# Kernel tuning notes

Hardware: AMD Instinct MI355X
Metric: run time of the kernel (lower is better)

Reference implementation:

```python
import jax, jax.numpy as jnp
import numpy as np

B, N, PD = 4, 4096, 1024
D, S = 16, 64              # max_span, span_dim
ALL = D * S                # 1024

# fwd[t, tau] = tau - t if 0 <= tau - t < D else D (points at padding slot)
FWD = np.array([[tau - t if 0 <= tau - t < D else D for tau in range(2 * D)]
                for t in range(D)], dtype=np.int32)           # [D, 2D]
BWD = np.array([[t + d for d in range(D)] for t in range(D)], dtype=np.int32)  # [D, D]
T_IDX = np.arange(D, dtype=np.int32)


def _gather(x, idx, padding):
    # x: [B, N, D, S]; pad span dim, reshape seq into blocks of D, gather spans.
    # out[b, n, t, j, s] = x_padded[b, n, t, idx[t, j], s]  -> [B, N//D, D, idx.shape[1], S]
    b, n, d, s = x.shape
    pad = jnp.full((b, n, 1, s), padding, dtype=x.dtype)
    x = jnp.concatenate([x, pad], axis=2).reshape(b, n // d, d, d + 1, s)
    return x[:, :, T_IDX[:, None], idx, :]


def setup_inputs() -> dict:
    key = jax.random.key(0)
    k1, k2, k3, k4, k5 = jax.random.split(key, 5)
    return {
        "x":   jax.random.normal(k1, (B, N, PD), jnp.float32),
        "W_r": jax.random.normal(k2, (PD, 2 * ALL), jnp.float32) * 0.02,
        "b_r": jax.random.normal(k3, (2 * ALL,), jnp.float32) * 0.02,
        "W_w": jax.random.normal(k4, (ALL, PD), jnp.float32) * 0.02,
        "b_w": jax.random.normal(k5, (PD,), jnp.float32) * 0.02,
    }


def reference(x, W_r, b_r, W_w, b_w):
    # reader: Linear(PD -> 2*ALL), split into left/right span logits
    P = (x @ W_r + b_r).reshape(B, N, 2, D, S)
    L = P[:, :, 0]                                  # [B, N, D, S]
    R = jnp.roll(P[:, :, 1], -1, axis=1)            # roll(-1) along seq
    Lg = _gather(L, FWD, -10000.0)                  # [B, T, D, 2D, S]
    Rg = _gather(R, np.roll(FWD, 1, axis=1), 0.0)   # [B, T, D, 2D, S]
    Lg = jnp.transpose(Lg, (0, 1, 4, 2, 3))         # [B, T, S, D, 2D]
    Rg = jnp.transpose(Rg, (0, 1, 4, 2, 3))
    Lg = jax.nn.softmax(Lg, axis=-1)
    L0, L1 = Lg[..., :D], Lg[..., D:]
    R0, R1 = Rg[..., :D], Rg[..., D:]
    Q0 = L0 @ R0                                    # [B, T, S, D, D]
    Q1 = L0 @ R1 + L1 @ jnp.roll(R0, -1, axis=1)
    mask = jnp.ones((Q1.shape[1],), Q1.dtype).at[-1].set(0.0)  # zero last block
    Q1 = Q1 * mask[None, :, None, None, None]
    Q = jnp.concatenate([Q0, Q1], axis=-1)          # [B, T, S, D, 2D]
    Q = jnp.transpose(Q, (0, 1, 3, 4, 2))           # [B, T, D, 2D, S]
    Q = Q[:, :, T_IDX[:, None], BWD, :]             # [B, T, D, D, S]
    out = Q.reshape(B, N, ALL)
    return out @ W_w + b_w                          # writer: Linear(ALL -> PD)
```

## Files before the change

kernel.cpp:

```cpp
#include <hip/hip_runtime.h>
#include <hip/hip_bf16.h>

#define B_ 4
#define N_ 4096
#define PD_ 1024
#define D_ 16
#define S_ 64
#define ALL_ 1024
#define TWOALL_ 2048
#define M_ 16384

typedef __bf16 bf16x8 __attribute__((ext_vector_type(8)));
typedef float floatx4 __attribute__((ext_vector_type(4)));

__device__ __forceinline__ float bf2f(unsigned short u) {
    union { unsigned int i; float f; } v;
    v.i = ((unsigned int)u) << 16;
    return v.f;
}

__device__ __forceinline__ unsigned short f2bf(float f) {
    unsigned int x = __float_as_uint(f);
    unsigned int r = (x + 0x7fffu + ((x >> 16) & 1u)) >> 16;
    return (unsigned short)r;
}

__device__ __forceinline__ void load_lds_16(const void* g, void* l) {
    __builtin_amdgcn_global_load_lds(
        (const __attribute__((address_space(1))) void*)g,
        (__attribute__((address_space(3))) void*)l, 16, 0, 0);
}

__global__ __launch_bounds__(256) void convert_f32_bf16(
    const float* __restrict__ in, unsigned short* __restrict__ out, int n4) {
    int i = blockIdx.x * 256 + threadIdx.x;
    if (i >= n4) return;
    float4 v = *(const float4*)(in + (size_t)i * 4);
    ushort4 o;
    o.x = f2bf(v.x); o.y = f2bf(v.y); o.z = f2bf(v.z); o.w = f2bf(v.w);
    *(ushort4*)(out + (size_t)i * 4) = o;
}

__global__ void transpose_f32_bf16(const float* __restrict__ in,
                                   unsigned short* __restrict__ out,
                                   int rows, int cols) {
    __shared__ float tile[32][33];
    int bx = blockIdx.x * 32;
    int by = blockIdx.y * 32;
    int tx = threadIdx.x;
    int ty = threadIdx.y;
    #pragma unroll
    for (int i = 0; i < 32; i += 8)
        tile[ty + i][tx] = in[(size_t)(by + ty + i) * cols + bx + tx];
    __syncthreads();
    #pragma unroll
    for (int i = 0; i < 32; i += 8)
        out[(size_t)(bx + ty + i) * rows + by + tx] = f2bf(tile[tx][ty + i]);
}

#define BM 256
#define BN 256
#define BK 64

#define STAGE_A(buf_, h_, kt_) do { \
    load_lds_16(a_base + (size_t)((h_) * 128) * K + (kt_) * 64, \
                &As[buf_][((h_) * 128 + wave * 16) * 64]); \
    load_lds_16(a_base + (size_t)((h_) * 128 + 8) * K + (kt_) * 64, \
                &As[buf_][((h_) * 128 + wave * 16 + 8) * 64]); \
  } while (0)

#define STAGE_B(buf_, h_, kt_) do { \
    load_lds_16(b_base + (size_t)((h_) * 128) * K + (kt_) * 64, \
                &Bs[buf_][((h_) * 128 + wave * 16) * 64]); \
    load_lds_16(b_base + (size_t)((h_) * 128 + 8) * K + (kt_) * 64, \
                &Bs[buf_][((h_) * 128 + wave * 16 + 8) * 64]); \
  } while (0)

#define LOAD_AF(mh_) do { \
    _Pragma("unroll") \
    for (int i = 0; i < 4; ++i) { \
        const unsigned short* p_ = Ab + (wm * 128 + (mh_) * 64 + i * 16 + lrow) * 64; \
        af[i][0] = *(const bf16x8*)(p_ + ((g0 ^ (lrow & 7)) * 8)); \
        af[i][1] = *(const bf16x8*)(p_ + (((g0 + 4) ^ (lrow & 7)) * 8)); \
    } } while (0)

#define LOAD_BH(dst_, nh_) do { \
    _Pragma("unroll") \
    for (int j = 0; j < 2; ++j) { \
        const unsigned short* p_ = Bb + (wn * 64 + (nh_) * 32 + j * 16 + lrow) * 64; \
        dst_[j][0] = *(const bf16x8*)(p_ + ((g0 ^ (lrow & 7)) * 8)); \
        dst_[j][1] = *(const bf16x8*)(p_ + (((g0 + 4) ^ (lrow & 7)) * 8)); \
    } } while (0)

#define MMA_Q(mh_, nh_, bq_) do { \
    __builtin_amdgcn_s_setprio(1); \
    _Pragma("unroll") \
    for (int kk = 0; kk < 2; ++kk) \
      _Pragma("unroll") \
      for (int i = 0; i < 4; ++i) \
        _Pragma("unroll") \
        for (int j = 0; j < 2; ++j) \
          acc[(mh_) * 4 + i][(nh_) * 2 + j] = \
              __builtin_amdgcn_mfma_f32_16x16x32_bf16( \
                  af[i][kk], bq_[j][kk], acc[(mh_) * 4 + i][(nh_) * 2 + j], 0, 0, 0); \
    __builtin_amdgcn_s_setprio(0); \
  } while (0)

#define MID_BAR() do { \
    __builtin_amdgcn_sched_barrier(0); \
    __builtin_amdgcn_s_barrier(); \
    asm volatile("s_waitcnt lgkmcnt(0)" ::: "memory"); \
  } while (0)

#define POST_BAR() do { \
    __builtin_amdgcn_s_barrier(); \
    __builtin_amdgcn_sched_barrier(0); \
  } while (0)

template <int OUT_BF>
__global__ __launch_bounds__(512, 2) void gemm_bf16(
    const unsigned short* __restrict__ A,
    const unsigned short* __restrict__ Bt,
    const float* __restrict__ bias,
    void* __restrict__ Cv,
    int M, int N, int K, int gxl, int gypx) {

    __shared__ __align__(16) unsigned short As[2][BM * BK];
    __shared__ __align__(16) unsigned short Bs[2][BN * BK];

    const int tid  = threadIdx.x;
    const int lane = tid & 63;
    const int wave = tid >> 6;
    const int wm   = wave & 1;
    const int wn   = wave >> 1;

    const int flat = blockIdx.x;
    const int xcd  = flat & 7;
    const int slot = flat >> 3;
    const int bx   = slot & ((1 << gxl) - 1);
    const int by   = xcd * gypx + (slot >> gxl);
    const int bm0  = by * BM;
    const int bn0  = bx * BN;

    const int lrow = lane & 15;
    const int g0   = lane >> 4;

    const int srow = lane >> 3;
    const int sg   = (lane & 7) ^ srow;

    const unsigned short* a_base =
        A + (size_t)(bm0 + wave * 16 + srow) * K + sg * 8;
    const unsigned short* b_base =
        Bt + (size_t)(bn0 + wave * 16 + srow) * K + sg * 8;

    floatx4 acc[8][4] = {};
    bf16x8 af[4][2];
    bf16x8 bf0[2][2];
    bf16x8 bf1[2][2];

    const int NTk = K >> 6;

    STAGE_A(0, 0, 0); STAGE_A(0, 1, 0); STAGE_B(0, 0, 0); STAGE_B(0, 1, 0);
    if (NTk > 1) {
        STAGE_A(1, 0, 1); STAGE_A(1, 1, 1); STAGE_B(1, 0, 1);
        asm volatile("s_waitcnt vmcnt(6)" ::: "memory");
    } else {
        asm volatile("s_waitcnt vmcnt(0)" ::: "memory");
    }
    POST_BAR();

    for (int t = 0; t < NTk; ++t) {
        const int buf = t & 1;
        const unsigned short* Ab = As[buf];
        const unsigned short* Bb = Bs[buf];

        LOAD_AF(0);
        LOAD_BH(bf0, 0);
        if (t + 1 < NTk) STAGE_B((t + 1) & 1, 1, t + 1);
        asm volatile("s_waitcnt lgkmcnt(8)" ::: "memory");
        MID_BAR();
        MMA_Q(0, 0, bf0);
        POST_BAR();

        LOAD_BH(bf1, 1);
        MID_BAR();
        MMA_Q(0, 1, bf1);
        POST_BAR();

        LOAD_AF(1);
        if (t + 2 < NTk) STAGE_B(buf, 0, t + 2);
        MID_BAR();
        MMA_Q(1, 1, bf1);
        POST_BAR();

        if (t + 2 < NTk) { STAGE_A(buf, 0, t + 2); STAGE_A(buf, 1, t + 2); }
        __builtin_amdgcn_sched_barrier(0);
        __builtin_amdgcn_s_barrier();
        MMA_Q(1, 0, bf0);
        if (t + 2 < NTk) {
            asm volatile("s_waitcnt vmcnt(6)" ::: "memory");
        } else if (t + 1 < NTk) {
            asm volatile("s_waitcnt vmcnt(0)" ::: "memory");
        }
        POST_BAR();
    }

    #pragma unroll
    for (int n = 0; n < 4; ++n) {
        int col = bn0 + wn * 64 + n * 16 + (lane & 15);
        float bv = bias[col];
        #pragma unroll
        for (int m = 0; m < 8; ++m) {
            #pragma unroll
            for (int r = 0; r < 4; ++r) {
                int row = bm0 + wm * 128 + m * 16 + (lane >> 4) * 4 + r;
                float v = acc[m][n][r] + bv;
                if (OUT_BF)
                    ((unsigned short*)Cv)[(size_t)row * N + col] = f2bf(v);
                else
                    ((float*)Cv)[(size_t)row * N + col] = v;
            }
        }
    }
}

__global__ __launch_bounds__(256) void middle_kernel(
    const unsigned short* __restrict__ P,
    unsigned short* __restrict__ A2) {

    int idx = blockIdx.x * 256 + threadIdx.x;
    int s   = idx & 63;
    int r   = idx >> 6;
    int n   = r & (N_ - 1);
    const int t = n & (D_ - 1);
    const int c = n >> 4;

    const unsigned short* Lp = P + (size_t)r * TWOALL_ + s;
    float w[16];
    float mx = -1e30f;
    #pragma unroll
    for (int j = 0; j < 16; ++j) {
        w[j] = bf2f(Lp[j * S_]);
        mx = fmaxf(mx, w[j]);
    }
    float sum = 0.f;
    #pragma unroll
    for (int j = 0; j < 16; ++j) {
        w[j] = __expf(w[j] - mx);
        sum += w[j];
    }
    float inv = 1.0f / sum;

    float q[16];
    #pragma unroll
    for (int d = 0; d < 16; ++d) q[d] = 0.f;

    #pragma unroll
    for (int i = 0; i < 15; ++i) {
        int np = n + i + 1;
        if (np >= N_) np -= N_;
        int b = r >> 12;
        const unsigned short* Rp = P + (((size_t)(b * N_ + np)) * 2 + 1) * ALL_ + s;
        #pragma unroll
        for (int k = 0; k < 15 - i; ++k) {
            q[i + k + 1] += w[i] * bf2f(Rp[k * S_]);
        }
    }

    unsigned short* out = A2 + (size_t)r * ALL_ + s;
    bool last = (c == (N_ / D_) - 1);
    #pragma unroll
    for (int d = 0; d < 16; ++d) {
        float v = (d == 0) ? 0.f : q[d] * inv;
        if (last && (t + d >= D_)) v = 0.f;
        out[d * S_] = f2bf(v);
    }
}

extern "C" void kernel_launch(void* const* d_in, const int* in_sizes, int n_in,
                              void* d_out, int out_size, void* d_ws, size_t ws_size,
                              hipStream_t stream) {
    const float* x   = (const float*)d_in[0];
    const float* W_r = (const float*)d_in[1];
    const float* b_r = (const float*)d_in[2];
    const float* W_w = (const float*)d_in[3];
    const float* b_w = (const float*)d_in[4];
    float* out = (float*)d_out;

    unsigned short* ws  = (unsigned short*)d_ws;
    unsigned short* P   = ws;
    unsigned short* xbf = P   + (size_t)M_ * TWOALL_;
    unsigned short* A2  = xbf + (size_t)M_ * ALL_;
    unsigned short* WrT = A2  + (size_t)M_ * ALL_;
    unsigned short* WwT = WrT + (size_t)TWOALL_ * PD_;

    convert_f32_bf16<<<dim3((M_ * PD_ / 4 + 255) / 256), 256, 0, stream>>>(
        x, xbf, M_ * PD_ / 4);

    dim3 tb(32, 8);
    transpose_f32_bf16<<<dim3(TWOALL_ / 32, PD_ / 32), tb, 0, stream>>>(W_r, WrT, PD_, TWOALL_);
    transpose_f32_bf16<<<dim3(ALL_ / 32, PD_ / 32), tb, 0, stream>>>(W_w, WwT, PD_, ALL_);

    gemm_bf16<1><<<dim3((TWOALL_ / BN) * (M_ / BM)), 512, 0, stream>>>(
        xbf, WrT, b_r, P, M_, TWOALL_, PD_, 3, (M_ / BM) / 8);

    middle_kernel<<<dim3((B_ * N_ * S_) / 256), 256, 0, stream>>>(P, A2);

    gemm_bf16<0><<<dim3((ALL_ / BN) * (M_ / BM)), 512, 0, stream>>>(
        A2, WwT, b_w, out, M_, ALL_, PD_, 2, (M_ / BM) / 8);
}
```

Baseline: 293.1 us.

## Restructure GEMM main loop prefetch schedule with one-ahead A and two-ahead B staging

Reorders the four MFMA quadrants so the A fragments are reloaded instead of holding two B fragment sets, which cuts register use. A tiles are now prefetched one K-step ahead into the opposite buffer and B tiles two steps ahead. Global and LDS addresses are precomputed as incrementing pointers and fixed offsets, and an extra scheduling barrier is added after the LDS wait. The cost is one additional LDS read of the A fragments per iteration, and the more intricate buffer hazard timing could stall or race.

```diff
diff --git a/kernel.cpp b/kernel.cpp
--- a/kernel.cpp
+++ b/kernel.cpp
@@ -62,47 +62,31 @@
 #define BN 256
 #define BK 64
 
-#define STAGE_A(buf_, h_, kt_) do { \
-    load_lds_16(a_base + (size_t)((h_) * 128) * K + (kt_) * 64, \
-                &As[buf_][((h_) * 128 + wave * 16) * 64]); \
-    load_lds_16(a_base + (size_t)((h_) * 128 + 8) * K + (kt_) * 64, \
-                &As[buf_][((h_) * 128 + wave * 16 + 8) * 64]); \
-  } while (0)
-
-#define STAGE_B(buf_, h_, kt_) do { \
-    load_lds_16(b_base + (size_t)((h_) * 128) * K + (kt_) * 64, \
-                &Bs[buf_][((h_) * 128 + wave * 16) * 64]); \
-    load_lds_16(b_base + (size_t)((h_) * 128 + 8) * K + (kt_) * 64, \
-                &Bs[buf_][((h_) * 128 + wave * 16 + 8) * 64]); \
-  } while (0)
-
 #define LOAD_AF(mh_) do { \
     _Pragma("unroll") \
-    for (int i = 0; i < 4; ++i) { \
-        const unsigned short* p_ = Ab + (wm * 128 + (mh_) * 64 + i * 16 + lrow) * 64; \
-        af[i][0] = *(const bf16x8*)(p_ + ((g0 ^ (lrow & 7)) * 8)); \
-        af[i][1] = *(const bf16x8*)(p_ + (((g0 + 4) ^ (lrow & 7)) * 8)); \
+    for (int i_ = 0; i_ < 4; ++i_) { \
+        af[i_][0] = *(const bf16x8*)(rdA + bufoff + (mh_) * 4096 + i_ * 1024 + cg0); \
+        af[i_][1] = *(const bf16x8*)(rdA + bufoff + (mh_) * 4096 + i_ * 1024 + cg1); \
     } } while (0)
 
-#define LOAD_BH(dst_, nh_) do { \
+#define LOAD_B(nh_) do { \
     _Pragma("unroll") \
-    for (int j = 0; j < 2; ++j) { \
-        const unsigned short* p_ = Bb + (wn * 64 + (nh_) * 32 + j * 16 + lrow) * 64; \
-        dst_[j][0] = *(const bf16x8*)(p_ + ((g0 ^ (lrow & 7)) * 8)); \
-        dst_[j][1] = *(const bf16x8*)(p_ + (((g0 + 4) ^ (lrow & 7)) * 8)); \
+    for (int j_ = 0; j_ < 2; ++j_) { \
+        bq[j_][0] = *(const bf16x8*)(rdB + bufoff + (nh_) * 2048 + j_ * 1024 + cg0); \
+        bq[j_][1] = *(const bf16x8*)(rdB + bufoff + (nh_) * 2048 + j_ * 1024 + cg1); \
     } } while (0)
 
-#define MMA_Q(mh_, nh_, bq_) do { \
+#define MMA_Q(mh_, nh_) do { \
     __builtin_amdgcn_s_setprio(1); \
     _Pragma("unroll") \
     for (int kk = 0; kk < 2; ++kk) \
       _Pragma("unroll") \
-      for (int i = 0; i < 4; ++i) \
+      for (int i_ = 0; i_ < 4; ++i_) \
         _Pragma("unroll") \
-        for (int j = 0; j < 2; ++j) \
-          acc[(mh_) * 4 + i][(nh_) * 2 + j] = \
+        for (int j_ = 0; j_ < 2; ++j_) \
+          acc[(mh_) * 4 + i_][(nh_) * 2 + j_] = \
               __builtin_amdgcn_mfma_f32_16x16x32_bf16( \
-                  af[i][kk], bq_[j][kk], acc[(mh_) * 4 + i][(nh_) * 2 + j], 0, 0, 0); \
+                  af[i_][kk], bq[j_][kk], acc[(mh_) * 4 + i_][(nh_) * 2 + j_], 0, 0, 0); \
     __builtin_amdgcn_s_setprio(0); \
   } while (0)
 
@@ -110,6 +94,7 @@
     __builtin_amdgcn_sched_barrier(0); \
     __builtin_amdgcn_s_barrier(); \
     asm volatile("s_waitcnt lgkmcnt(0)" ::: "memory"); \
+    __builtin_amdgcn_sched_barrier(0); \
   } while (0)
 
 #define POST_BAR() do { \
@@ -153,56 +138,97 @@
     const unsigned short* b_base =
         Bt + (size_t)(bn0 + wave * 16 + srow) * K + sg * 8;
 
+    const int cg0 = (g0 ^ (lrow & 7)) * 8;
+    const int cg1 = cg0 ^ 32;
+    const unsigned short* rdA = &As[0][(wm * 128 + lrow) * 64];
+    const unsigned short* rdB = &Bs[0][(wn * 64  + lrow) * 64];
+
+    const unsigned short* pA0  = a_base + 64;
+    const unsigned short* pA0b = a_base + 64 + (size_t)8   * K;
+    const unsigned short* pA1  = a_base + 64 + (size_t)128 * K;
+    const unsigned short* pA1b = a_base + 64 + (size_t)136 * K;
+    const unsigned short* pB0  = b_base + 128;
+    const unsigned short* pB0b = b_base + 128 + (size_t)8   * K;
+    const unsigned short* pB1  = b_base + 128 + (size_t)128 * K;
+    const unsigned short* pB1b = b_base + 128 + (size_t)136 * K;
+
     floatx4 acc[8][4] = {};
     bf16x8 af[4][2];
-    bf16x8 bf0[2][2];
-    bf16x8 bf1[2][2];
+    bf16x8 bq[2][2];
 
     const int NTk = K >> 6;
 
-    STAGE_A(0, 0, 0); STAGE_A(0, 1, 0); STAGE_B(0, 0, 0); STAGE_B(0, 1, 0);
-    if (NTk > 1) {
-        STAGE_A(1, 0, 1); STAGE_A(1, 1, 1); STAGE_B(1, 0, 1);
-        asm volatile("s_waitcnt vmcnt(6)" ::: "memory");
-    } else {
-        asm volatile("s_waitcnt vmcnt(0)" ::: "memory");
+    {
+        unsigned short* d0 = &As[0][wave * 1024];
+        load_lds_16(a_base,                      d0);
+        load_lds_16(a_base + (size_t)8   * K,    d0 + 512);
+        load_lds_16(a_base + (size_t)128 * K,    d0 + 8192);
+        load_lds_16(a_base + (size_t)136 * K,    d0 + 8704);
+        unsigned short* d1 = &Bs[0][wave * 1024];
+        load_lds_16(b_base,                      d1);
+        load_lds_16(b_base + (size_t)8   * K,    d1 + 512);
+        load_lds_16(b_base + (size_t)128 * K,    d1 + 8192);
+        load_lds_16(b_base + (size_t)136 * K,    d1 + 8704);
+        if (NTk > 1) {
+            unsigned short* d2 = &Bs[1][wave * 1024];
+            load_lds_16(b_base + 64,                    d2);
+            load_lds_16(b_base + 64 + (size_t)8   * K,  d2 + 512);
+            load_lds_16(b_base + 64 + (size_t)128 * K,  d2 + 8192);
+            load_lds_16(b_base + 64 + (size_t)136 * K,  d2 + 8704);
+            asm volatile("s_waitcnt vmcnt(4)" ::: "memory");
+        } else {
+            asm volatile("s_waitcnt vmcnt(0)" ::: "memory");
+        }
     }
     POST_BAR();
 
     for (int t = 0; t < NTk; ++t) {
-        const int buf = t & 1;
-        const unsigned short* Ab = As[buf];
-        const unsigned short* Bb = Bs[buf];
+        const int bufoff = (t & 1) << 14;
+        unsigned short* dA = &As[(t & 1) ^ 1][wave * 1024];
+        unsigned short* dB = &Bs[t & 1][wave * 1024];
 
         LOAD_AF(0);
-        LOAD_BH(bf0, 0);
-        if (t + 1 < NTk) STAGE_B((t + 1) & 1, 1, t + 1);
-        asm volatile("s_waitcnt lgkmcnt(8)" ::: "memory");
+        LOAD_B(0);
+        if (t + 1 < NTk) {
+            load_lds_16(pA0,  dA);
+            load_lds_16(pA0b, dA + 512);
+        }
         MID_BAR();
-        MMA_Q(0, 0, bf0);
+        MMA_Q(0, 0);
         POST_BAR();
 
-        LOAD_BH(bf1, 1);
+        LOAD_AF(1);
+        if (t + 1 < NTk) {
+            load_lds_16(pA1,  dA + 8192);
+            load_lds_16(pA1b, dA + 8704);
+        }
         MID_BAR();
-        MMA_Q(0, 1, bf1);
+        MMA_Q(1, 0);
         POST_BAR();
 
-        LOAD_AF(1);
-        if (t + 2 < NTk) STAGE_B(buf, 0, t + 2);
+        LOAD_B(1);
         MID_BAR();
-        MMA_Q(1, 1, bf1);
+        MMA_Q(1, 1);
         POST_BAR();
 
-        if (t + 2 < NTk) { STAGE_A(buf, 0, t + 2); STAGE_A(buf, 1, t + 2); }
-        __builtin_amdgcn_sched_barrier(0);
-        __builtin_amdgcn_s_barrier();
-        MMA_Q(1, 0, bf0);
+        LOAD_AF(0);
         if (t + 2 < NTk) {
-            asm volatile("s_waitcnt vmcnt(6)" ::: "memory");
+            load_lds_16(pB0,  dB);
+            load_lds_16(pB0b, dB + 512);
+            load_lds_16(pB1,  dB + 8192);
+            load_lds_16(pB1b, dB + 8704);
+        }
+        MID_BAR();
+        MMA_Q(0, 1);
+        if (t + 2 < NTk) {
+            asm volatile("s_waitcnt vmcnt(4)" ::: "memory");
         } else if (t + 1 < NTk) {
             asm volatile("s_waitcnt vmcnt(0)" ::: "memory");
         }
         POST_BAR();
+
+        pA0 += 64; pA0b += 64; pA1 += 64; pA1b += 64;
+        pB0 += 64; pB0b += 64; pB1 += 64; pB1b += 64;
     }
 
     #pragma unroll
```

Result: no change. 296.5 us (+1.2%).
